# Optimization experiments

Measured on AMD Instinct MI355X. Metric: run time of the kernel, lower is better.

The kernel has to match this reference:

```python
import jax, jax.numpy as jnp
import numpy as np

N_NODES = 100000
N_EDGES = 3200000
BATCH = 16
HIDDEN = 64


def setup_inputs() -> dict:
    key = jax.random.key(0)
    k_mu, k_ei, k_w1, k_b1, k_w2, k_b2 = jax.random.split(key, 6)
    mu = jax.random.normal(k_mu, (BATCH, N_NODES), dtype=jnp.float32)
    edge_index = jax.random.randint(k_ei, (2, N_EDGES), 0, N_NODES, dtype=jnp.int64)
    # MLP params: Linear(1, hidden) -> GELU -> Linear(hidden, 1)
    W1 = jax.random.normal(k_w1, (1, HIDDEN), dtype=jnp.float32) * (1.0 / np.sqrt(1))
    b1 = jax.random.normal(k_b1, (HIDDEN,), dtype=jnp.float32) * 0.02
    W2 = jax.random.normal(k_w2, (HIDDEN, 1), dtype=jnp.float32) * (1.0 / np.sqrt(HIDDEN))
    b2 = jax.random.normal(k_b2, (1,), dtype=jnp.float32) * 0.02
    return {"mu": mu, "edge_index": edge_index, "W1": W1, "b1": b1, "W2": W2, "b2": b2}


def reference(mu, edge_index, W1, b1, W2, b2):
    row, col = edge_index[0], edge_index[1]
    B, N = mu.shape
    # degree of each destination node (clamped at 1)
    deg = jax.ops.segment_sum(jnp.ones_like(row, dtype=mu.dtype), row, num_segments=N)
    deg = jnp.maximum(deg, 1.0)  # [N]
    # batched message aggregation: gather source values, scatter-add to rows
    msgs = mu[:, col].T                                    # [E, B]
    agg = jax.ops.segment_sum(msgs, row, num_segments=N)   # [N, B]
    out = agg.T / deg[None, :]                             # [B, N]
    # tiny MLP applied per scalar: 1 -> hidden -> 1 with exact (erf) GELU
    h = jax.nn.gelu(out[..., None] * W1[0][None, None, :] + b1, approximate=False)  # [B, N, H]
    y = jnp.einsum('bnh,h->bn', h, W2[:, 0]) + b2[0]       # [B, N]
    return y
```

## Files before the change

kernel.cpp:

```cpp
#include <hip/hip_runtime.h>
#include <hip/hip_fp16.h>

#define N_NODES 100000
#define N_EDGES 3200000
#define BATCH   16
#define HIDDEN  64

#define NBINS   512
#define NPB     196
#define CAP_BIN 7168
#define EPB     8192
#define MAXW    14

#define PBLKS   391
#define TBLKS   196
#define LBLKS   17

#define LUT_SIZE  8192
#define LUT_LO    (-16.0f)
#define LUT_SCALE (LUT_SIZE / 32.0f)

typedef int v4i __attribute__((ext_vector_type(4)));

__global__ __launch_bounds__(512) void fused_part_prep_kernel(
    const int* __restrict__ ei, unsigned int* __restrict__ gcnt,
    unsigned int* __restrict__ packed,
    const float* __restrict__ mu, __half* __restrict__ mu_h,
    const float* __restrict__ W1, const float* __restrict__ b1,
    const float* __restrict__ W2, const float* __restrict__ b2,
    float* __restrict__ lut) {
  __shared__ int aux[NBINS];
  __shared__ int wsum[8];
  __shared__ unsigned int stag[EPB];
  __shared__ unsigned short sbin[EPB];

  int blk = blockIdx.x;
  int t = threadIdx.x;

  if (blk >= PBLKS) {
    if (blk < PBLKS + TBLKS) {
      int n = (blk - PBLKS) * 512 + t;
      if (n >= N_NODES) return;
      float4 o[4];
#pragma unroll
      for (int q = 0; q < 4; ++q) {
        o[q].x = mu[(q * 4 + 0) * N_NODES + n];
        o[q].y = mu[(q * 4 + 1) * N_NODES + n];
        o[q].z = mu[(q * 4 + 2) * N_NODES + n];
        o[q].w = mu[(q * 4 + 3) * N_NODES + n];
      }
      __half2 hh[8];
#pragma unroll
      for (int q = 0; q < 4; ++q) {
        hh[2 * q]     = __floats2half2_rn(o[q].x, o[q].y);
        hh[2 * q + 1] = __floats2half2_rn(o[q].z, o[q].w);
      }
      int4 w0 = make_int4(*(int*)&hh[0], *(int*)&hh[1], *(int*)&hh[2], *(int*)&hh[3]);
      int4 w1 = make_int4(*(int*)&hh[4], *(int*)&hh[5], *(int*)&hh[6], *(int*)&hh[7]);
      int4* dst = (int4*)(mu_h + (size_t)n * BATCH);
      dst[0] = w0;
      dst[1] = w1;
    } else {
      int i = (blk - PBLKS - TBLKS) * 512 + t;
      if (i > LUT_SIZE) return;
      float x = LUT_LO + (float)i / LUT_SCALE;
      float acc = b2[0];
      for (int h = 0; h < HIDDEN; ++h) {
        float z = fmaf(x, W1[h], b1[h]);
        float g = 0.5f * z * (1.0f + erff(z * 0.70710678118654752f));
        acc = fmaf(g, W2[h], acc);
      }
      lut[i] = acc;
    }
    return;
  }

  int base = blk * EPB;
  int nvalid = min(EPB, N_EDGES - base);
  aux[t] = 0;
  __syncthreads();

  unsigned int pk[16];
  int bn[16];
  int rk[16];
  if (t * 16 + 16 <= nvalid) {
    const v4i* rp = (const v4i*)(ei + base + t * 16);
    const v4i* cp = (const v4i*)(ei + N_EDGES + base + t * 16);
    v4i rr[4], cc[4];
#pragma unroll
    for (int q = 0; q < 4; ++q) {
      rr[q] = __builtin_nontemporal_load(&rp[q]);
      cc[q] = __builtin_nontemporal_load(&cp[q]);
    }
#pragma unroll
    for (int q = 0; q < 4; ++q) {
#pragma unroll
      for (int u = 0; u < 4; ++u) {
        int k = q * 4 + u;
        int r = rr[q][u];
        int c = cc[q][u];
        int b = r / NPB;
        int rl = r - b * NPB;
        pk[k] = ((unsigned int)rl << 17) | (unsigned int)c;
        bn[k] = b;
      }
    }
#pragma unroll
    for (int k = 0; k < 16; ++k) rk[k] = atomicAdd(&aux[bn[k]], 1);
  } else {
#pragma unroll
    for (int k = 0; k < 16; ++k) {
      int e = t * 16 + k;
      if (e < nvalid) {
        int r = ei[base + e];
        int c = ei[N_EDGES + base + e];
        int b = r / NPB;
        int rl = r - b * NPB;
        pk[k] = ((unsigned int)rl << 17) | (unsigned int)c;
        bn[k] = b;
        rk[k] = atomicAdd(&aux[b], 1);
      } else {
        bn[k] = -1;
      }
    }
  }
  __syncthreads();

  int lane = t & 63;
  int wid = t >> 6;
  int v = aux[t];

  unsigned int gb = v ? atomicAdd(&gcnt[t], (unsigned int)v) : 0u;

  int sv = v;
#pragma unroll
  for (int d = 1; d < 64; d <<= 1) {
    int n = __shfl_up(sv, d, 64);
    if (lane >= d) sv += n;
  }
  if (lane == 63) wsum[wid] = sv;
  __syncthreads();
  if (t < 8) {
    int s = wsum[t];
#pragma unroll
    for (int d = 1; d < 8; d <<= 1) {
      int n = __shfl_up(s, d, 8);
      if (t >= d) s += n;
    }
    wsum[t] = s;
  }
  __syncthreads();
  int pexcl = sv + (wid ? wsum[wid - 1] : 0) - v;
  aux[t] = pexcl;
  __syncthreads();

#pragma unroll
  for (int k = 0; k < 16; ++k) {
    if (bn[k] >= 0) {
      int p = aux[bn[k]] + rk[k];
      stag[p] = pk[k];
      sbin[p] = (unsigned short)bn[k];
    }
  }
  __syncthreads();

  aux[t] = (int)gb - pexcl;
  __syncthreads();

  for (int i = t; i < nvalid; i += 512) {
    int b = sbin[i];
    unsigned int pos = (unsigned int)(i + aux[b]);
    if (pos < CAP_BIN)
      __builtin_nontemporal_store(stag[i], &packed[(size_t)b * CAP_BIN + pos]);
  }
}

__global__ __launch_bounds__(512) void scatter_apply_kernel(
    const unsigned int* __restrict__ gcnt, const unsigned int* __restrict__ packed,
    const __half* __restrict__ mu_h, const float* __restrict__ lut,
    float* __restrict__ out) {
  __shared__ unsigned int scol[CAP_BIN];
  __shared__ int dcnt[NPB];
  __shared__ int ebase[NPB];
  __shared__ int wpart[4];

  int t = threadIdx.x;
  int bin = blockIdx.x;

  int cnt = min((int)gcnt[bin], CAP_BIN);
  const unsigned int* pp = packed + (size_t)bin * CAP_BIN;

  if (t < NPB) dcnt[t] = 0;
  __syncthreads();

  unsigned int w[MAXW];
#pragma unroll
  for (int k = 0; k < MAXW; ++k) w[k] = pp[k * 512 + t];

  int rk[MAXW];
#pragma unroll
  for (int k = 0; k < MAXW; ++k) {
    int i = k * 512 + t;
    rk[k] = (i < cnt) ? atomicAdd(&dcnt[w[k] >> 17], 1) : 0;
  }
  __syncthreads();

  int v = 0, sv = 0;
  if (t < 256) {
    v = (t < NPB) ? dcnt[t] : 0;
    int lane = t & 63;
    sv = v;
#pragma unroll
    for (int d = 1; d < 64; d <<= 1) {
      int n = __shfl_up(sv, d, 64);
      if (lane >= d) sv += n;
    }
    if (lane == 63) wpart[t >> 6] = sv;
  }
  __syncthreads();
  if (t < 256) {
    int wid = t >> 6;
    int off = 0;
#pragma unroll
    for (int q = 0; q < 3; ++q)
      if (wid > q) off += wpart[q];
    if (t < NPB) ebase[t] = sv + off - v;
  }
  __syncthreads();

#pragma unroll
  for (int k = 0; k < MAXW; ++k) {
    int i = k * 512 + t;
    if (i < cnt) {
      int rl = (int)(w[k] >> 17);
      scol[ebase[rl] + rk[k]] = w[k] & 0x1FFFFu;
    }
  }
  __syncthreads();

  const __half2* mu2 = (const __half2*)mu_h;
  int j2 = t & 7;
  int nsl = t >> 3;
  int binBase = bin * NPB;

#pragma unroll
  for (int pass = 0; pass < 4; ++pass) {
    int nl = pass * 64 + nsl;
    if (nl < NPB) {
      int node = binBase + nl;
      if (node < N_NODES) {
        int s = ebase[nl];
        int e = s + dcnt[nl];
        float2 a0 = {0.f, 0.f}, a1 = {0.f, 0.f};
        float2 a2 = {0.f, 0.f}, a3 = {0.f, 0.f};
        int i = s;
        for (; i + 4 <= e; i += 4) {
          int c0 = (int)scol[i];
          int c1 = (int)scol[i + 1];
          int c2 = (int)scol[i + 2];
          int c3 = (int)scol[i + 3];
          __half2 v0 = mu2[(size_t)c0 * 8 + j2];
          __half2 v1 = mu2[(size_t)c1 * 8 + j2];
          __half2 v2 = mu2[(size_t)c2 * 8 + j2];
          __half2 v3 = mu2[(size_t)c3 * 8 + j2];
          float2 f0 = __half22float2(v0);
          float2 f1 = __half22float2(v1);
          float2 f2 = __half22float2(v2);
          float2 f3 = __half22float2(v3);
          a0.x += f0.x; a0.y += f0.y;
          a1.x += f1.x; a1.y += f1.y;
          a2.x += f2.x; a2.y += f2.y;
          a3.x += f3.x; a3.y += f3.y;
        }
        for (; i < e; ++i) {
          float2 f = __half22float2(mu2[(size_t)scol[i] * 8 + j2]);
          a0.x += f.x; a0.y += f.y;
        }
        float sx = (a0.x + a1.x) + (a2.x + a3.x);
        float sy = (a0.y + a1.y) + (a2.y + a3.y);
        float dinv = 1.0f / (float)max(e - s, 1);

        float xs[2] = {sx * dinv, sy * dinv};
#pragma unroll
        for (int q = 0; q < 2; ++q) {
          float u = (xs[q] - LUT_LO) * LUT_SCALE;
          u = fminf(fmaxf(u, 0.0f), (float)LUT_SIZE - 0.001f);
          int ii = (int)u;
          float frac = u - (float)ii;
          float lo = lut[ii];
          float hi = lut[ii + 1];
          __builtin_nontemporal_store(fmaf(hi - lo, frac, lo),
                                      &out[(size_t)(2 * j2 + q) * N_NODES + node]);
        }
      }
    }
  }
}

extern "C" void kernel_launch(void* const* d_in, const int* in_sizes, int n_in,
                              void* d_out, int out_size, void* d_ws, size_t ws_size,
                              hipStream_t stream) {
  const float* mu = (const float*)d_in[0];
  const int*   ei = (const int*)d_in[1];
  const float* W1 = (const float*)d_in[2];
  const float* b1 = (const float*)d_in[3];
  const float* W2 = (const float*)d_in[4];
  const float* b2 = (const float*)d_in[5];
  float* out = (float*)d_out;

  __half* mu_h = (__half*)d_ws;
  float* lut  = (float*)(mu_h + (size_t)N_NODES * BATCH);
  unsigned int* gcnt = (unsigned int*)(lut + LUT_SIZE + 1);
  unsigned int* packed = gcnt + NBINS;

  (void)hipMemsetAsync(gcnt, 0, NBINS * sizeof(unsigned int), stream);

  fused_part_prep_kernel<<<PBLKS + TBLKS + LBLKS, 512, 0, stream>>>(
      ei, gcnt, packed, mu, mu_h, W1, b1, W2, b2, lut);

  scatter_apply_kernel<<<NBINS, 512, 0, stream>>>(gcnt, packed, mu_h, lut, out);
}
```

Baseline: 134.7 us.

## Halve bin size to 98 nodes and double bin count for more blocks

Doubles the number of destination bins to 1024, each covering 98 nodes with half the capacity, and halves the edges per partition block. Each partition thread now handles two bins, and the scatter kernel needs only two passes and a two-wave scan. Launch bounds request four blocks per CU, and packed loads become nontemporal. The goal is to cut LDS and register use per block so more blocks fit on each CU and the 256 CUs get more parallel work. The cost is more global atomics on the bin counters and more partition blocks, each doing the same per-block overhead.

```diff
diff --git a/kernel.cpp b/kernel.cpp
--- a/kernel.cpp
+++ b/kernel.cpp
@@ -6,13 +6,13 @@
 #define BATCH   16
 #define HIDDEN  64
 
-#define NBINS   512
-#define NPB     196
-#define CAP_BIN 7168
-#define EPB     8192
-#define MAXW    14
-
-#define PBLKS   391
+#define NBINS   1024
+#define NPB     98
+#define CAP_BIN 3584
+#define EPB     4096
+#define MAXW    7
+
+#define PBLKS   782
 #define TBLKS   196
 #define LBLKS   17
 
@@ -22,7 +22,7 @@
 
 typedef int v4i __attribute__((ext_vector_type(4)));
 
-__global__ __launch_bounds__(512) void fused_part_prep_kernel(
+__global__ __launch_bounds__(512, 4) void fused_part_prep_kernel(
     const int* __restrict__ ei, unsigned int* __restrict__ gcnt,
     unsigned int* __restrict__ packed,
     const float* __restrict__ mu, __half* __restrict__ mu_h,
@@ -77,23 +77,24 @@
 
   int base = blk * EPB;
   int nvalid = min(EPB, N_EDGES - base);
-  aux[t] = 0;
-  __syncthreads();
-
-  unsigned int pk[16];
-  int bn[16];
-  int rk[16];
-  if (t * 16 + 16 <= nvalid) {
-    const v4i* rp = (const v4i*)(ei + base + t * 16);
-    const v4i* cp = (const v4i*)(ei + N_EDGES + base + t * 16);
-    v4i rr[4], cc[4];
-#pragma unroll
-    for (int q = 0; q < 4; ++q) {
+  aux[2 * t] = 0;
+  aux[2 * t + 1] = 0;
+  __syncthreads();
+
+  unsigned int pk[8];
+  int bn[8];
+  int rk[8];
+  if (t * 8 + 8 <= nvalid) {
+    const v4i* rp = (const v4i*)(ei + base + t * 8);
+    const v4i* cp = (const v4i*)(ei + N_EDGES + base + t * 8);
+    v4i rr[2], cc[2];
+#pragma unroll
+    for (int q = 0; q < 2; ++q) {
       rr[q] = __builtin_nontemporal_load(&rp[q]);
       cc[q] = __builtin_nontemporal_load(&cp[q]);
     }
 #pragma unroll
-    for (int q = 0; q < 4; ++q) {
+    for (int q = 0; q < 2; ++q) {
 #pragma unroll
       for (int u = 0; u < 4; ++u) {
         int k = q * 4 + u;
@@ -106,11 +107,11 @@
       }
     }
 #pragma unroll
-    for (int k = 0; k < 16; ++k) rk[k] = atomicAdd(&aux[bn[k]], 1);
+    for (int k = 0; k < 8; ++k) rk[k] = atomicAdd(&aux[bn[k]], 1);
   } else {
 #pragma unroll
-    for (int k = 0; k < 16; ++k) {
-      int e = t * 16 + k;
+    for (int k = 0; k < 8; ++k) {
+      int e = t * 8 + k;
       if (e < nvalid) {
         int r = ei[base + e];
         int c = ei[N_EDGES + base + e];
@@ -128,9 +129,12 @@
 
   int lane = t & 63;
   int wid = t >> 6;
-  int v = aux[t];
-
-  unsigned int gb = v ? atomicAdd(&gcnt[t], (unsigned int)v) : 0u;
+  int c0 = aux[2 * t];
+  int c1 = aux[2 * t + 1];
+  int v = c0 + c1;
+
+  unsigned int gb0 = c0 ? atomicAdd(&gcnt[2 * t], (unsigned int)c0) : 0u;
+  unsigned int gb1 = c1 ? atomicAdd(&gcnt[2 * t + 1], (unsigned int)c1) : 0u;
 
   int sv = v;
 #pragma unroll
@@ -151,11 +155,14 @@
   }
   __syncthreads();
   int pexcl = sv + (wid ? wsum[wid - 1] : 0) - v;
-  aux[t] = pexcl;
-  __syncthreads();
-
-#pragma unroll
-  for (int k = 0; k < 16; ++k) {
+  int p0 = pexcl;
+  int p1 = pexcl + c0;
+  aux[2 * t] = p0;
+  aux[2 * t + 1] = p1;
+  __syncthreads();
+
+#pragma unroll
+  for (int k = 0; k < 8; ++k) {
     if (bn[k] >= 0) {
       int p = aux[bn[k]] + rk[k];
       stag[p] = pk[k];
@@ -164,7 +171,8 @@
   }
   __syncthreads();
 
-  aux[t] = (int)gb - pexcl;
+  aux[2 * t] = (int)gb0 - p0;
+  aux[2 * t + 1] = (int)gb1 - p1;
   __syncthreads();
 
   for (int i = t; i < nvalid; i += 512) {
@@ -175,14 +183,14 @@
   }
 }
 
-__global__ __launch_bounds__(512) void scatter_apply_kernel(
+__global__ __launch_bounds__(512, 4) void scatter_apply_kernel(
     const unsigned int* __restrict__ gcnt, const unsigned int* __restrict__ packed,
     const __half* __restrict__ mu_h, const float* __restrict__ lut,
     float* __restrict__ out) {
   __shared__ unsigned int scol[CAP_BIN];
   __shared__ int dcnt[NPB];
   __shared__ int ebase[NPB];
-  __shared__ int wpart[4];
+  __shared__ int wpart[2];
 
   int t = threadIdx.x;
   int bin = blockIdx.x;
@@ -195,7 +203,7 @@
 
   unsigned int w[MAXW];
 #pragma unroll
-  for (int k = 0; k < MAXW; ++k) w[k] = pp[k * 512 + t];
+  for (int k = 0; k < MAXW; ++k) w[k] = __builtin_nontemporal_load(&pp[k * 512 + t]);
 
   int rk[MAXW];
 #pragma unroll
@@ -206,7 +214,7 @@
   __syncthreads();
 
   int v = 0, sv = 0;
-  if (t < 256) {
+  if (t < 128) {
     v = (t < NPB) ? dcnt[t] : 0;
     int lane = t & 63;
     sv = v;
@@ -218,12 +226,8 @@
     if (lane == 63) wpart[t >> 6] = sv;
   }
   __syncthreads();
-  if (t < 256) {
-    int wid = t >> 6;
-    int off = 0;
-#pragma unroll
-    for (int q = 0; q < 3; ++q)
-      if (wid > q) off += wpart[q];
+  if (t < 128) {
+    int off = (t >= 64) ? wpart[0] : 0;
     if (t < NPB) ebase[t] = sv + off - v;
   }
   __syncthreads();
@@ -244,7 +248,7 @@
   int binBase = bin * NPB;
 
 #pragma unroll
-  for (int pass = 0; pass < 4; ++pass) {
+  for (int pass = 0; pass < 2; ++pass) {
     int nl = pass * 64 + nsl;
     if (nl < NPB) {
       int node = binBase + nl;
```

Result: slower. 159.0 us (+18.0%).

## Shard per-bin global counters into sub-buckets and unroll gather loop by eight

Applied to the files above, without the earlier changes.

Each destination bin's global atomic counter is split into 8 shards, chosen by partition block index. Each shard owns a fixed 1024-slot region of the bin's packed buffer, which cuts same-address atomic contention between partition blocks. The scatter kernel reads the per-shard counts and validates each loaded word against its shard's count. Bin capacity grows to 8192 slots, so every bin loads more, possibly empty, slots. The gather loop also gains an 8-way unrolled body to raise memory-level parallelism. A shard that receives more than 1024 edges would silently drop them, and the extra unroll adds register pressure.

```diff
diff --git a/kernel.cpp b/kernel.cpp
--- a/kernel.cpp
+++ b/kernel.cpp
@@ -8,9 +8,11 @@
 
 #define NBINS   512
 #define NPB     196
-#define CAP_BIN 7168
+#define NSH     8
+#define CAP_SH  1024
+#define CAP_BIN 8192
 #define EPB     8192
-#define MAXW    14
+#define MAXW    16
 
 #define PBLKS   391
 #define TBLKS   196
@@ -77,6 +79,7 @@
 
   int base = blk * EPB;
   int nvalid = min(EPB, N_EDGES - base);
+  int sh = blk & (NSH - 1);
   aux[t] = 0;
   __syncthreads();
 
@@ -130,7 +133,7 @@
   int wid = t >> 6;
   int v = aux[t];
 
-  unsigned int gb = v ? atomicAdd(&gcnt[t], (unsigned int)v) : 0u;
+  unsigned int gb = v ? atomicAdd(&gcnt[t * NSH + sh], (unsigned int)v) : 0u;
 
   int sv = v;
 #pragma unroll
@@ -164,13 +167,14 @@
   }
   __syncthreads();
 
-  aux[t] = (int)gb - pexcl;
-  __syncthreads();
-
+  aux[t] = (int)(sh * CAP_SH + gb) - pexcl;
+  __syncthreads();
+
+  unsigned int lim = (unsigned int)((sh + 1) * CAP_SH);
   for (int i = t; i < nvalid; i += 512) {
     int b = sbin[i];
     unsigned int pos = (unsigned int)(i + aux[b]);
-    if (pos < CAP_BIN)
+    if (pos < lim)
       __builtin_nontemporal_store(stag[i], &packed[(size_t)b * CAP_BIN + pos]);
   }
 }
@@ -183,14 +187,15 @@
   __shared__ int dcnt[NPB];
   __shared__ int ebase[NPB];
   __shared__ int wpart[4];
+  __shared__ int scnt_s[NSH];
 
   int t = threadIdx.x;
   int bin = blockIdx.x;
 
-  int cnt = min((int)gcnt[bin], CAP_BIN);
   const unsigned int* pp = packed + (size_t)bin * CAP_BIN;
 
   if (t < NPB) dcnt[t] = 0;
+  if (t < NSH) scnt_s[t] = min((int)gcnt[bin * NSH + t], CAP_SH);
   __syncthreads();
 
   unsigned int w[MAXW];
@@ -200,8 +205,8 @@
   int rk[MAXW];
 #pragma unroll
   for (int k = 0; k < MAXW; ++k) {
-    int i = k * 512 + t;
-    rk[k] = (i < cnt) ? atomicAdd(&dcnt[w[k] >> 17], 1) : 0;
+    int off = ((k & 1) << 9) + t;
+    rk[k] = (off < scnt_s[k >> 1]) ? atomicAdd(&dcnt[w[k] >> 17], 1) : 0;
   }
   __syncthreads();
 
@@ -230,8 +235,8 @@
 
 #pragma unroll
   for (int k = 0; k < MAXW; ++k) {
-    int i = k * 512 + t;
-    if (i < cnt) {
+    int off = ((k & 1) << 9) + t;
+    if (off < scnt_s[k >> 1]) {
       int rl = (int)(w[k] >> 17);
       scol[ebase[rl] + rk[k]] = w[k] & 0x1FFFFu;
     }
@@ -254,6 +259,36 @@
         float2 a0 = {0.f, 0.f}, a1 = {0.f, 0.f};
         float2 a2 = {0.f, 0.f}, a3 = {0.f, 0.f};
         int i = s;
+        for (; i + 8 <= e; i += 8) {
+          int c0 = (int)scol[i];
+          int c1 = (int)scol[i + 1];
+          int c2 = (int)scol[i + 2];
+          int c3 = (int)scol[i + 3];
+          int c4 = (int)scol[i + 4];
+          int c5 = (int)scol[i + 5];
+          int c6 = (int)scol[i + 6];
+          int c7 = (int)scol[i + 7];
+          __half2 v0 = mu2[(size_t)c0 * 8 + j2];
+          __half2 v1 = mu2[(size_t)c1 * 8 + j2];
+          __half2 v2 = mu2[(size_t)c2 * 8 + j2];
+          __half2 v3 = mu2[(size_t)c3 * 8 + j2];
+          __half2 v4 = mu2[(size_t)c4 * 8 + j2];
+          __half2 v5 = mu2[(size_t)c5 * 8 + j2];
+          __half2 v6 = mu2[(size_t)c6 * 8 + j2];
+          __half2 v7 = mu2[(size_t)c7 * 8 + j2];
+          float2 f0 = __half22float2(v0);
+          float2 f1 = __half22float2(v1);
+          float2 f2 = __half22float2(v2);
+          float2 f3 = __half22float2(v3);
+          float2 f4 = __half22float2(v4);
+          float2 f5 = __half22float2(v5);
+          float2 f6 = __half22float2(v6);
+          float2 f7 = __half22float2(v7);
+          a0.x += f0.x + f4.x; a0.y += f0.y + f4.y;
+          a1.x += f1.x + f5.x; a1.y += f1.y + f5.y;
+          a2.x += f2.x + f6.x; a2.y += f2.y + f6.y;
+          a3.x += f3.x + f7.x; a3.y += f3.y + f7.y;
+        }
         for (; i + 4 <= e; i += 4) {
           int c0 = (int)scol[i];
           int c1 = (int)scol[i + 1];
@@ -311,9 +346,9 @@
   __half* mu_h = (__half*)d_ws;
   float* lut  = (float*)(mu_h + (size_t)N_NODES * BATCH);
   unsigned int* gcnt = (unsigned int*)(lut + LUT_SIZE + 1);
-  unsigned int* packed = gcnt + NBINS;
-
-  (void)hipMemsetAsync(gcnt, 0, NBINS * sizeof(unsigned int), stream);
+  unsigned int* packed = gcnt + NBINS * NSH;
+
+  (void)hipMemsetAsync(gcnt, 0, NBINS * NSH * sizeof(unsigned int), stream);
 
   fused_part_prep_kernel<<<PBLKS + TBLKS + LBLKS, 512, 0, stream>>>(
       ei, gcnt, packed, mu, mu_h, W1, b1, W2, b2, lut);
```

New measurement: 130.4 us. 3.2% less time.
